# Optimization experiments

Hardware: AMD Instinct MI355X
Metric: run time of the kernel (lower is better)

## Reference

```python
import jax, jax.numpy as jnp
import numpy as np

B, T = 64, 1024
ATTN_DIM, RNN_DIM, ENC_DIM = 128, 1024, 512
N_FILT, KSIZE = 32, 31
PAD = (KSIZE - 1) // 2


def setup_inputs() -> dict:
    key = jax.random.key(0)
    ks = jax.random.split(key, 11)
    query = jax.random.normal(ks[0], (B, RNN_DIM), dtype=jnp.float32)
    keys = jax.random.normal(ks[1], (B, T, ENC_DIM), dtype=jnp.float32)
    values = jax.random.normal(ks[2], (B, T, ENC_DIM), dtype=jnp.float32)
    attention_weights_cum = jax.random.uniform(ks[3], (B, T), dtype=jnp.float32)
    mask = jnp.zeros((B, T), dtype=bool)
    s = 0.02
    W_loc_conv = jax.random.normal(ks[4], (N_FILT, 1, KSIZE), dtype=jnp.float32) * s
    W_loc_proj = jax.random.normal(ks[5], (ATTN_DIM, N_FILT), dtype=jnp.float32) * s
    W_query = jax.random.normal(ks[6], (ATTN_DIM, RNN_DIM), dtype=jnp.float32) * s
    W_key = jax.random.normal(ks[7], (ATTN_DIM, ENC_DIM), dtype=jnp.float32) * s
    W_value = jax.random.normal(ks[8], (ENC_DIM, ENC_DIM), dtype=jnp.float32) * s
    W_attn = jax.random.normal(ks[9], (1, ATTN_DIM), dtype=jnp.float32) * s
    return {
        "query": query, "keys": keys, "values": values,
        "attention_weights_cum": attention_weights_cum, "mask": mask,
        "W_loc_conv": W_loc_conv, "W_loc_proj": W_loc_proj,
        "W_query": W_query, "W_key": W_key, "W_value": W_value, "W_attn": W_attn,
    }


def reference(query, keys, values, attention_weights_cum, mask,
              W_loc_conv, W_loc_proj, W_query, W_key, W_value, W_attn):
    # location features: conv1d over cumulative attention, (B,1,T) -> (B,N_FILT,T)
    loc = jax.lax.conv_general_dilated(
        attention_weights_cum[:, None, :], W_loc_conv,
        window_strides=(1,), padding=[(PAD, PAD)],
        dimension_numbers=("NCH", "OIH", "NCH"))
    # (B,T,N_FILT) @ W_loc_proj.T -> (B,T,ATTN_DIM)
    loc_feat = jnp.einsum("bft,af->bta", loc, W_loc_proj)
    q_proj = query @ W_query.T                      # (B, ATTN_DIM)
    k_proj = jnp.einsum("bte,ae->bta", keys, W_key)  # (B, T, ATTN_DIM)
    energies = jnp.tanh(q_proj[:, None, :] + k_proj + loc_feat)
    scores = jnp.einsum("bta,a->bt", energies, W_attn[0])  # (B, T)
    scores = jnp.where(mask, -jnp.inf, scores)
    attn = jax.nn.softmax(scores, axis=-1)
    v_proj = jnp.einsum("bte,fe->btf", values, W_value)  # (B, T, ENC_DIM)
    context = jnp.einsum("bt,btf->bf", attn, v_proj)      # (B, ENC_DIM)
    return context, attn
```

## Files before the change

kernel.cpp:

```cpp
#include <hip/hip_runtime.h>
#include <math.h>

#define B_   64
#define T_   1024
#define AD   128
#define RD   1024
#define ED   512
#define NF   32
#define KS   31
#define PADW 15

typedef short bf16x8 __attribute__((ext_vector_type(8)));
typedef float f32x4  __attribute__((ext_vector_type(4)));

typedef __attribute__((address_space(1))) unsigned gu32;
typedef __attribute__((address_space(3))) unsigned lu32;

__device__ __forceinline__ void gll16(const void* g, void* l) {
  __builtin_amdgcn_global_load_lds(
      (gu32*)(unsigned long long)g,
      (lu32*)(unsigned)(unsigned long long)l, 16, 0, 0);
}

__device__ __forceinline__ short f2bf(float x) {
  union { float f; unsigned u; } v; v.f = x;
  unsigned r = (v.u + 0x7FFFu + ((v.u >> 16) & 1u)) >> 16;
  return (short)r;
}

__device__ __forceinline__ float tanh_fast(float x) {
  float t = __expf(2.0f * x);
  return (t - 1.0f) * __builtin_amdgcn_rcpf(t + 1.0f);
}

#define WAITV_(n)  asm volatile("s_waitcnt vmcnt(" #n ")" ::: "memory")
#define WAITV(n)   WAITV_(n)
#define WAITVL_(n) asm volatile("s_waitcnt vmcnt(" #n ") lgkmcnt(0)" ::: "memory")
#define WAITVL(n)  WAITVL_(n)
#define SB  __builtin_amdgcn_sched_barrier(0)
#define BAR __builtin_amdgcn_s_barrier()

__global__ __launch_bounds__(256) void prep_kernel(
    const float* __restrict__ Wk, const float* __restrict__ Wlp,
    const float* __restrict__ awc, const float* __restrict__ Wc,
    const float* __restrict__ query, const float* __restrict__ Wq,
    short* __restrict__ Wk16, short* __restrict__ Wlp16,
    short* __restrict__ loc_g, float* __restrict__ qp) {
  __shared__ float sh_awc[128 + KS - 1];
  __shared__ float sh_wc[NF * KS];
  __shared__ float sh_q[RD];
  __shared__ float sh_red[AD];
  const int blk = blockIdx.x, tid = threadIdx.x;

  if (blk < 68) {
    int p = blk * 256 + tid;
    const float* src; short* dst; int off;
    if (p < 16384) { src = Wk; dst = Wk16; off = p; }
    else           { src = Wlp; dst = Wlp16; off = p - 16384; }
    float4 v = *(const float4*)&src[off * 4];
    short4 h = { f2bf(v.x), f2bf(v.y), f2bf(v.z), f2bf(v.w) };
    *(short4*)&dst[off * 4] = h;
  } else if (blk < 68 + 512) {
    int cb = blk - 68;
    int b = cb >> 3, t0 = (cb & 7) * 128;
    for (int i = tid; i < NF * KS; i += 256) sh_wc[i] = Wc[i];
    if (tid < 128 + KS - 1) {
      int gt = t0 - PADW + tid;
      sh_awc[tid] = (gt >= 0 && gt < T_) ? awc[b * T_ + gt] : 0.0f;
    }
    __syncthreads();
    const int t = tid & 127, fh = (tid >> 7) * 16;
    for (int fq = 0; fq < 4; ++fq) {
      float s0 = 0.f, s1 = 0.f, s2 = 0.f, s3 = 0.f;
      const float* w0 = &sh_wc[(fh + fq * 4 + 0) * KS];
      const float* w1 = &sh_wc[(fh + fq * 4 + 1) * KS];
      const float* w2 = &sh_wc[(fh + fq * 4 + 2) * KS];
      const float* w3 = &sh_wc[(fh + fq * 4 + 3) * KS];
#pragma unroll
      for (int k = 0; k < KS; ++k) {
        float aw = sh_awc[t + k];
        s0 += w0[k] * aw; s1 += w1[k] * aw; s2 += w2[k] * aw; s3 += w3[k] * aw;
      }
      short4 h = { f2bf(s0), f2bf(s1), f2bf(s2), f2bf(s3) };
      *(short4*)&loc_g[((size_t)(b * T_ + t0 + t)) * NF + fh + fq * 4] = h;
    }
  } else {
    int b = blk - (68 + 512);
    *(float4*)&sh_q[tid * 4] = *(const float4*)&query[b * RD + tid * 4];
    __syncthreads();
    const int a = tid & 127, kh = tid >> 7;
    const float* wr = &Wq[(size_t)a * RD + kh * 512];
    const float* qr = &sh_q[kh * 512];
    float acc = 0.f;
    for (int e = 0; e < 512; e += 4) {
      float4 w = *(const float4*)&wr[e];
      acc += w.x * qr[e] + w.y * qr[e + 1] + w.z * qr[e + 2] + w.w * qr[e + 3];
    }
    if (kh == 1) sh_red[a] = acc;
    __syncthreads();
    if (kh == 0) qp[b * AD + a] = acc + sh_red[a];
  }
}

__global__ __launch_bounds__(256, 2) void scores_kernel(
    const float* __restrict__ keys, const short* __restrict__ Wk16,
    const short* __restrict__ Wlp16, const short* __restrict__ loc_g,
    const float* __restrict__ qp, const float* __restrict__ Wa,
    float* __restrict__ scores) {
  __shared__ alignas(16) short As[128 * 64];
  __shared__ alignas(16) short Bs[2][128 * 64];
  __shared__ float qp_s[AD], wa_s[AD];
  __shared__ float sc_s[128 * 2];

  const int tid = threadIdx.x;
  const int b = blockIdx.y, t0 = blockIdx.x * 128;
  const int lane = tid & 63, wave = tid >> 6;
  const int wm = wave >> 1, wn = wave & 1;
  const int m16 = lane & 15, s4 = lane >> 4;

  const int sr = tid >> 3;
  const int sg = tid & 7;
  const int swz = (sg ^ (sr & 7)) * 8;
  const float* kA = &keys[((size_t)(b * T_ + t0 + sr)) * ED + sg * 8];

  float4 bufA[8], bufB[8];
  auto LOADA = [&](float4 (&buf)[8], int kc) {
#pragma unroll
    for (int i = 0; i < 4; ++i) {
      const float* p = kA + (size_t)i * 32 * ED + (size_t)kc * 64;
      buf[2 * i]     = *(const float4*)p;
      buf[2 * i + 1] = *(const float4*)(p + 4);
    }
  };
  auto WRITEA = [&](float4 (&buf)[8]) {
#pragma unroll
    for (int i = 0; i < 4; ++i) {
      bf16x8 h = { f2bf(buf[2*i].x),   f2bf(buf[2*i].y),
                   f2bf(buf[2*i].z),   f2bf(buf[2*i].w),
                   f2bf(buf[2*i+1].x), f2bf(buf[2*i+1].y),
                   f2bf(buf[2*i+1].z), f2bf(buf[2*i+1].w) };
      *(bf16x8*)&As[(sr + i * 32) * 64 + swz] = h;
    }
  };

  const int r8 = lane >> 3, cb8 = lane & 7;
  const int cbg = cb8 ^ r8;
  auto STAGEB = [&](int kc, int half) {
#pragma unroll
    for (int i = 0; i < 4; ++i) {
      int row = wave * 32 + i * 8;
      gll16(&Wk16[(size_t)(row + r8) * ED + (size_t)kc * 64 + cbg * 8],
            &Bs[half][row * 64]);
    }
  };
  f32x4 acc[4][4];
  auto COMPUTE = [&](int half) {
#pragma unroll
    for (int kk2 = 0; kk2 < 2; ++kk2) {
      const int j = kk2 * 4 + s4;
      const int ca = (j ^ (m16 & 7)) * 8;
      bf16x8 af[4], bfr[4];
#pragma unroll
      for (int mt = 0; mt < 4; ++mt)
        af[mt] = *(const bf16x8*)&As[(wm * 64 + mt * 16 + m16) * 64 + ca];
#pragma unroll
      for (int nt = 0; nt < 4; ++nt)
        bfr[nt] = *(const bf16x8*)&Bs[half][(wn * 64 + nt * 16 + m16) * 64 + ca];
      __builtin_amdgcn_s_setprio(1);
#pragma unroll
      for (int mt = 0; mt < 4; ++mt)
#pragma unroll
        for (int nt = 0; nt < 4; ++nt)
          acc[mt][nt] = __builtin_amdgcn_mfma_f32_16x16x32_bf16(
              af[mt], bfr[nt], acc[mt][nt], 0, 0, 0);
      __builtin_amdgcn_s_setprio(0);
    }
  };

  if (tid < AD) qp_s[tid] = qp[b * AD + tid];
  else          wa_s[tid - AD] = Wa[tid - AD];
  SB;
  {
    const int r = lane >> 2, cbl = lane & 3;
#pragma unroll
    for (int i = 0; i < 2; ++i) {
      int row = wave * 32 + i * 16;
      gll16(&loc_g[((size_t)(b * T_ + t0 + row + r)) * NF + cbl * 8],
            &As[row * 32]);
      gll16(&Wlp16[(row + r) * NF + cbl * 8], &Bs[1][row * 32]);
    }
  }
  SB;
  LOADA(bufA, 0); SB;
  STAGEB(0, 0);   SB;
  LOADA(bufB, 1); SB;
  WAITVL(20);
  SB; BAR; SB;

  {
    bf16x8 af[4], bfr[4];
#pragma unroll
    for (int mt = 0; mt < 4; ++mt)
      af[mt] = *(const bf16x8*)&As[(wm * 64 + mt * 16 + m16) * 32 + s4 * 8];
#pragma unroll
    for (int nt = 0; nt < 4; ++nt)
      bfr[nt] = *(const bf16x8*)&Bs[1][(wn * 64 + nt * 16 + m16) * 32 + s4 * 8];
#pragma unroll
    for (int mt = 0; mt < 4; ++mt)
#pragma unroll
      for (int nt = 0; nt < 4; ++nt)
        acc[mt][nt] = __builtin_amdgcn_mfma_f32_16x16x32_bf16(
            af[mt], bfr[nt], (f32x4){0.f, 0.f, 0.f, 0.f}, 0, 0, 0);
  }

#define CHUNK(i, BUF, PRE, MID, DOG, DOL)                    \
  do {                                                       \
    BAR; SB;           \
    WAITV(PRE); SB;                     \
    WRITEA(BUF); SB;                                         \
    if (DOG) STAGEB((i) + 1, ((i) + 1) & 1);                 \
    SB;                                                      \
    if (DOL) LOADA(BUF, (i) + 2);                            \
    SB;                                                      \
    WAITVL(MID);            \
    SB; BAR; SB;                                             \
    COMPUTE((i) & 1);                                        \
  } while (0)

  CHUNK(0, bufA, 12, 20, true,  true);
  CHUNK(1, bufB, 12, 20, true,  true);
  CHUNK(2, bufA, 12, 20, true,  true);
  CHUNK(3, bufB, 12, 20, true,  true);
  CHUNK(4, bufA, 12, 20, true,  true);
  CHUNK(5, bufB, 12, 20, true,  true);
  CHUNK(6, bufA, 12, 12, true,  false);
  CHUNK(7, bufB,  4,  0, false, false);
#undef CHUNK

  __syncthreads();

  float qv[4], wv[4];
#pragma unroll
  for (int nt = 0; nt < 4; ++nt) {
    int a = wn * 64 + nt * 16 + m16;
    qv[nt] = qp_s[a]; wv[nt] = wa_s[a];
  }
#pragma unroll
  for (int mt = 0; mt < 4; ++mt) {
#pragma unroll
    for (int r = 0; r < 4; ++r) {
      float p = 0.f;
#pragma unroll
      for (int nt = 0; nt < 4; ++nt)
        p += wv[nt] * tanh_fast(acc[mt][nt][r] + qv[nt]);
      p += __shfl_xor(p, 1); p += __shfl_xor(p, 2);
      p += __shfl_xor(p, 4); p += __shfl_xor(p, 8);
      if (m16 == 0) sc_s[(wm * 64 + mt * 16 + s4 * 4 + r) * 2 + wn] = p;
    }
  }
  __syncthreads();
  if (tid < 128)
    scores[(size_t)b * T_ + t0 + tid] = sc_s[tid * 2] + sc_s[tid * 2 + 1];
}

__global__ __launch_bounds__(256) void softmax_kernel(
    const float* __restrict__ scores, const unsigned char* __restrict__ mask,
    float* __restrict__ attn) {
  const int b = blockIdx.x, tid = threadIdx.x;
  __shared__ float redm[4], reds[4];

  float4 s4 = *(const float4*)&scores[b * T_ + tid * 4];
  uchar4 m4 = *(const uchar4*)&mask[b * T_ + tid * 4];
  if (m4.x) s4.x = -INFINITY;
  if (m4.y) s4.y = -INFINITY;
  if (m4.z) s4.z = -INFINITY;
  if (m4.w) s4.w = -INFINITY;

  float mx = fmaxf(fmaxf(s4.x, s4.y), fmaxf(s4.z, s4.w));
#pragma unroll
  for (int off = 32; off >= 1; off >>= 1) mx = fmaxf(mx, __shfl_xor(mx, off, 64));
  if ((tid & 63) == 0) redm[tid >> 6] = mx;
  __syncthreads();
  mx = fmaxf(fmaxf(redm[0], redm[1]), fmaxf(redm[2], redm[3]));

  float e0 = expf(s4.x - mx), e1 = expf(s4.y - mx);
  float e2 = expf(s4.z - mx), e3 = expf(s4.w - mx);
  float sum = e0 + e1 + e2 + e3;
#pragma unroll
  for (int off = 32; off >= 1; off >>= 1) sum += __shfl_xor(sum, off, 64);
  if ((tid & 63) == 0) reds[tid >> 6] = sum;
  __syncthreads();
  sum = reds[0] + reds[1] + reds[2] + reds[3];

  float inv = 1.0f / sum;
  float4 o4 = { e0 * inv, e1 * inv, e2 * inv, e3 * inv };
  *(float4*)&attn[b * T_ + tid * 4] = o4;
}

__global__ __launch_bounds__(256) void wvsum_kernel(
    const float* __restrict__ values, const float* __restrict__ attn,
    float* __restrict__ wvp) {
  const int tc = blockIdx.x, b = blockIdx.y, tid = threadIdx.x;
  __shared__ float at_s[32];
  if (tid < 32) at_s[tid] = attn[b * T_ + tc * 32 + tid];
  __syncthreads();
  const int e4 = tid & 127, th = tid >> 7;
  const float* vb =
      values + ((size_t)(b * T_ + tc * 32 + th * 16)) * ED + e4 * 4;
  const float* as = &at_s[th * 16];
  float4 acc = {0.f, 0.f, 0.f, 0.f};
#pragma unroll
  for (int t8 = 0; t8 < 16; t8 += 8) {
    float4 v[8];
#pragma unroll
    for (int u = 0; u < 8; ++u)
      v[u] = *(const float4*)&vb[(size_t)(t8 + u) * ED];
#pragma unroll
    for (int u = 0; u < 8; ++u) {
      float a = as[t8 + u];
      acc.x = fmaf(a, v[u].x, acc.x); acc.y = fmaf(a, v[u].y, acc.y);
      acc.z = fmaf(a, v[u].z, acc.z); acc.w = fmaf(a, v[u].w, acc.w);
    }
  }
  *(float4*)&wvp[((size_t)(b * 64 + tc * 2 + th)) * ED + e4 * 4] = acc;
}

__global__ __launch_bounds__(256) void context_kernel(
    const float* __restrict__ wvp, const float* __restrict__ Wv,
    float* __restrict__ ctx) {
  const int fq = blockIdx.x, b = blockIdx.y, tid = threadIdx.x;
  __shared__ float wv_s[ED];
  __shared__ float red[128];
  for (int e = tid; e < ED; e += 256) {
    float s = 0.f;
    const float* base = &wvp[(size_t)b * 64 * ED + e];
#pragma unroll 16
    for (int p = 0; p < 64; ++p) s += base[p * ED];
    wv_s[e] = s;
  }
  __syncthreads();
  const int fl = tid & 127, eh = tid >> 7;
  const int f = fq * 128 + fl;
  const float* wr = &Wv[(size_t)f * ED + eh * 256];
  const float* qr = &wv_s[eh * 256];
  float acc = 0.f;
  for (int e = 0; e < 256; e += 4) {
    float4 w = *(const float4*)&wr[e];
    acc += w.x * qr[e] + w.y * qr[e + 1] + w.z * qr[e + 2] + w.w * qr[e + 3];
  }
  if (eh == 1) red[fl] = acc;
  __syncthreads();
  if (eh == 0) ctx[b * ED + f] = acc + red[fl];
}

extern "C" void kernel_launch(void* const* d_in, const int* in_sizes, int n_in,
                              void* d_out, int out_size, void* d_ws, size_t ws_size,
                              hipStream_t stream) {
  const float* query = (const float*)d_in[0];
  const float* keys  = (const float*)d_in[1];
  const float* values= (const float*)d_in[2];
  const float* awc   = (const float*)d_in[3];
  const unsigned char* mask = (const unsigned char*)d_in[4];
  const float* Wc    = (const float*)d_in[5];
  const float* Wlp   = (const float*)d_in[6];
  const float* Wq    = (const float*)d_in[7];
  const float* Wk    = (const float*)d_in[8];
  const float* Wv    = (const float*)d_in[9];
  const float* Wa    = (const float*)d_in[10];

  float* ctx  = (float*)d_out;
  float* attn = (float*)d_out + B_ * ED;

  float* ws = (float*)d_ws;
  float* qp      = ws;
  float* scoresB = qp + B_ * AD;
  float* wvp     = scoresB + B_ * T_;
  short* Wk16    = (short*)(wvp + (size_t)B_ * 64 * ED);
  short* Wlp16   = Wk16 + AD * ED;
  short* loc_g   = Wlp16 + AD * NF;

  prep_kernel<<<68 + 512 + 64, 256, 0, stream>>>(Wk, Wlp, awc, Wc, query, Wq,
                                                 Wk16, Wlp16, loc_g, qp);
  scores_kernel<<<dim3(8, B_), 256, 0, stream>>>(keys, Wk16, Wlp16, loc_g,
                                                 qp, Wa, scoresB);
  softmax_kernel<<<B_, 256, 0, stream>>>(scoresB, mask, attn);
  wvsum_kernel<<<dim3(32, B_), 256, 0, stream>>>(values, attn, wvp);
  context_kernel<<<dim3(4, B_), 256, 0, stream>>>(wvp, Wv, ctx);
}
```

Baseline: 338.4 us.

## Fuse softmax into scores and context into wvsum via last-block counters

Removes the separate softmax and context kernels. The last scores block for each batch, found with an atomic counter, computes the softmax. The weighted value sum now uses 8 blocks per batch that each cover 128 timesteps, with register double-buffered loads. Partial sums are combined by float atomics into a per-batch buffer, and the last block applies Wv to produce the context. This cuts two launches and the large wvp intermediate, at the cost of serial tail work in a single block per batch, fewer blocks for the value pass, and nondeterministic float atomic ordering.

```diff
diff --git a/kernel.cpp b/kernel.cpp
--- a/kernel.cpp
+++ b/kernel.cpp
@@ -45,7 +45,9 @@
     const float* __restrict__ awc, const float* __restrict__ Wc,
     const float* __restrict__ query, const float* __restrict__ Wq,
     short* __restrict__ Wk16, short* __restrict__ Wlp16,
-    short* __restrict__ loc_g, float* __restrict__ qp) {
+    short* __restrict__ loc_g, float* __restrict__ qp,
+    float* __restrict__ yb, int* __restrict__ cnt_sm,
+    int* __restrict__ cnt_wv) {
   __shared__ float sh_awc[128 + KS - 1];
   __shared__ float sh_wc[NF * KS];
   __shared__ float sh_q[RD];
@@ -86,6 +88,10 @@
     }
   } else {
     int b = blk - (68 + 512);
+    if (tid < 128) *(float4*)&yb[(size_t)b * ED + tid * 4] =
+        (float4){0.f, 0.f, 0.f, 0.f};
+    if (tid == 254) cnt_sm[b] = 0;
+    if (tid == 255) cnt_wv[b] = 0;
     *(float4*)&sh_q[tid * 4] = *(const float4*)&query[b * RD + tid * 4];
     __syncthreads();
     const int a = tid & 127, kh = tid >> 7;
@@ -106,11 +112,14 @@
     const float* __restrict__ keys, const short* __restrict__ Wk16,
     const short* __restrict__ Wlp16, const short* __restrict__ loc_g,
     const float* __restrict__ qp, const float* __restrict__ Wa,
-    float* __restrict__ scores) {
+    const unsigned char* __restrict__ mask, float* __restrict__ scores,
+    float* __restrict__ attn, int* __restrict__ cnt_sm) {
   __shared__ alignas(16) short As[128 * 64];
   __shared__ alignas(16) short Bs[2][128 * 64];
   __shared__ float qp_s[AD], wa_s[AD];
   __shared__ float sc_s[128 * 2];
+  __shared__ float redm[4], reds[4];
+  __shared__ int lastf;
 
   const int tid = threadIdx.x;
   const int b = blockIdx.y, t0 = blockIdx.x * 128;
@@ -261,30 +270,30 @@
   __syncthreads();
   if (tid < 128)
     scores[(size_t)b * T_ + t0 + tid] = sc_s[tid * 2] + sc_s[tid * 2 + 1];
-}
-
-__global__ __launch_bounds__(256) void softmax_kernel(
-    const float* __restrict__ scores, const unsigned char* __restrict__ mask,
-    float* __restrict__ attn) {
-  const int b = blockIdx.x, tid = threadIdx.x;
-  __shared__ float redm[4], reds[4];
-
-  float4 s4 = *(const float4*)&scores[b * T_ + tid * 4];
+
+  __threadfence();
+  __syncthreads();
+  if (tid == 0) lastf = (atomicAdd(&cnt_sm[b], 1) == 7) ? 1 : 0;
+  __syncthreads();
+  if (!lastf) return;
+  __threadfence();
+
+  float4 s4v = *(const float4*)&scores[(size_t)b * T_ + tid * 4];
   uchar4 m4 = *(const uchar4*)&mask[b * T_ + tid * 4];
-  if (m4.x) s4.x = -INFINITY;
-  if (m4.y) s4.y = -INFINITY;
-  if (m4.z) s4.z = -INFINITY;
-  if (m4.w) s4.w = -INFINITY;
-
-  float mx = fmaxf(fmaxf(s4.x, s4.y), fmaxf(s4.z, s4.w));
+  if (m4.x) s4v.x = -INFINITY;
+  if (m4.y) s4v.y = -INFINITY;
+  if (m4.z) s4v.z = -INFINITY;
+  if (m4.w) s4v.w = -INFINITY;
+
+  float mx = fmaxf(fmaxf(s4v.x, s4v.y), fmaxf(s4v.z, s4v.w));
 #pragma unroll
   for (int off = 32; off >= 1; off >>= 1) mx = fmaxf(mx, __shfl_xor(mx, off, 64));
   if ((tid & 63) == 0) redm[tid >> 6] = mx;
   __syncthreads();
   mx = fmaxf(fmaxf(redm[0], redm[1]), fmaxf(redm[2], redm[3]));
 
-  float e0 = expf(s4.x - mx), e1 = expf(s4.y - mx);
-  float e2 = expf(s4.z - mx), e3 = expf(s4.w - mx);
+  float e0 = expf(s4v.x - mx), e1 = expf(s4v.y - mx);
+  float e2 = expf(s4v.z - mx), e3 = expf(s4v.w - mx);
   float sum = e0 + e1 + e2 + e3;
 #pragma unroll
   for (int off = 32; off >= 1; off >>= 1) sum += __shfl_xor(sum, off, 64);
@@ -297,60 +306,79 @@
   *(float4*)&attn[b * T_ + tid * 4] = o4;
 }
 
-__global__ __launch_bounds__(256) void wvsum_kernel(
+__global__ __launch_bounds__(256) void wvctx_kernel(
     const float* __restrict__ values, const float* __restrict__ attn,
-    float* __restrict__ wvp) {
+    const float* __restrict__ Wv, float* __restrict__ yb,
+    int* __restrict__ cnt_wv, float* __restrict__ ctx) {
   const int tc = blockIdx.x, b = blockIdx.y, tid = threadIdx.x;
-  __shared__ float at_s[32];
-  if (tid < 32) at_s[tid] = attn[b * T_ + tc * 32 + tid];
-  __syncthreads();
+  __shared__ float at_s[128];
+  __shared__ float4 red[128];
+  __shared__ float y_s[ED];
+  __shared__ int lastw;
+
+  if (tid < 128) at_s[tid] = attn[b * T_ + tc * 128 + tid];
+  __syncthreads();
+
   const int e4 = tid & 127, th = tid >> 7;
   const float* vb =
-      values + ((size_t)(b * T_ + tc * 32 + th * 16)) * ED + e4 * 4;
-  const float* as = &at_s[th * 16];
+      values + ((size_t)(b * T_ + tc * 128 + th * 64)) * ED + e4 * 4;
+  const float* as = &at_s[th * 64];
+
   float4 acc = {0.f, 0.f, 0.f, 0.f};
-#pragma unroll
-  for (int t8 = 0; t8 < 16; t8 += 8) {
-    float4 v[8];
-#pragma unroll
-    for (int u = 0; u < 8; ++u)
-      v[u] = *(const float4*)&vb[(size_t)(t8 + u) * ED];
+  float4 cur[8], nxt[8];
+#pragma unroll
+  for (int u = 0; u < 8; ++u) cur[u] = *(const float4*)&vb[(size_t)u * ED];
+#pragma unroll
+  for (int t8 = 0; t8 < 64; t8 += 8) {
+    if (t8 + 8 < 64) {
+#pragma unroll
+      for (int u = 0; u < 8; ++u)
+        nxt[u] = *(const float4*)&vb[(size_t)(t8 + 8 + u) * ED];
+    }
 #pragma unroll
     for (int u = 0; u < 8; ++u) {
       float a = as[t8 + u];
-      acc.x = fmaf(a, v[u].x, acc.x); acc.y = fmaf(a, v[u].y, acc.y);
-      acc.z = fmaf(a, v[u].z, acc.z); acc.w = fmaf(a, v[u].w, acc.w);
-    }
-  }
-  *(float4*)&wvp[((size_t)(b * 64 + tc * 2 + th)) * ED + e4 * 4] = acc;
-}
-
-__global__ __launch_bounds__(256) void context_kernel(
-    const float* __restrict__ wvp, const float* __restrict__ Wv,
-    float* __restrict__ ctx) {
-  const int fq = blockIdx.x, b = blockIdx.y, tid = threadIdx.x;
-  __shared__ float wv_s[ED];
-  __shared__ float red[128];
-  for (int e = tid; e < ED; e += 256) {
-    float s = 0.f;
-    const float* base = &wvp[(size_t)b * 64 * ED + e];
-#pragma unroll 16
-    for (int p = 0; p < 64; ++p) s += base[p * ED];
-    wv_s[e] = s;
-  }
-  __syncthreads();
-  const int fl = tid & 127, eh = tid >> 7;
-  const int f = fq * 128 + fl;
-  const float* wr = &Wv[(size_t)f * ED + eh * 256];
-  const float* qr = &wv_s[eh * 256];
-  float acc = 0.f;
-  for (int e = 0; e < 256; e += 4) {
-    float4 w = *(const float4*)&wr[e];
-    acc += w.x * qr[e] + w.y * qr[e + 1] + w.z * qr[e + 2] + w.w * qr[e + 3];
-  }
-  if (eh == 1) red[fl] = acc;
-  __syncthreads();
-  if (eh == 0) ctx[b * ED + f] = acc + red[fl];
+      acc.x = fmaf(a, cur[u].x, acc.x); acc.y = fmaf(a, cur[u].y, acc.y);
+      acc.z = fmaf(a, cur[u].z, acc.z); acc.w = fmaf(a, cur[u].w, acc.w);
+    }
+#pragma unroll
+    for (int u = 0; u < 8; ++u) cur[u] = nxt[u];
+  }
+
+  if (th == 1) red[e4] = acc;
+  __syncthreads();
+  if (th == 0) {
+    float4 r = red[e4];
+    acc.x += r.x; acc.y += r.y; acc.z += r.z; acc.w += r.w;
+    float* yp = &yb[(size_t)b * ED + e4 * 4];
+    atomicAdd(yp + 0, acc.x); atomicAdd(yp + 1, acc.y);
+    atomicAdd(yp + 2, acc.z); atomicAdd(yp + 3, acc.w);
+  }
+
+  __threadfence();
+  __syncthreads();
+  if (tid == 0) lastw = (atomicAdd(&cnt_wv[b], 1) == 7) ? 1 : 0;
+  __syncthreads();
+  if (!lastw) return;
+  __threadfence();
+
+  if (tid < 128)
+    *(float4*)&y_s[tid * 4] = *(const float4*)&yb[(size_t)b * ED + tid * 4];
+  __syncthreads();
+
+  const int f0 = tid * 2;
+  const float* w0 = &Wv[(size_t)f0 * ED];
+  const float* w1 = w0 + ED;
+  float a0 = 0.f, a1 = 0.f;
+  for (int e = 0; e < ED; e += 4) {
+    float4 y = *(const float4*)&y_s[e];
+    float4 wA = *(const float4*)&w0[e];
+    float4 wB = *(const float4*)&w1[e];
+    a0 += wA.x * y.x + wA.y * y.y + wA.z * y.z + wA.w * y.w;
+    a1 += wB.x * y.x + wB.y * y.y + wB.z * y.z + wB.w * y.w;
+  }
+  ctx[(size_t)b * ED + f0]     = a0;
+  ctx[(size_t)b * ED + f0 + 1] = a1;
 }
 
 extern "C" void kernel_launch(void* const* d_in, const int* in_sizes, int n_in,
@@ -374,16 +402,17 @@
   float* ws = (float*)d_ws;
   float* qp      = ws;
   float* scoresB = qp + B_ * AD;
-  float* wvp     = scoresB + B_ * T_;
-  short* Wk16    = (short*)(wvp + (size_t)B_ * 64 * ED);
+  float* yb      = scoresB + B_ * T_;
+  int*   cnt_sm  = (int*)(yb + B_ * ED);
+  int*   cnt_wv  = cnt_sm + 64;
+  short* Wk16    = (short*)(cnt_sm + 128);
   short* Wlp16   = Wk16 + AD * ED;
   short* loc_g   = Wlp16 + AD * NF;
 
-  prep_kernel<<<68 + 512 + 64, 256, 0, stream>>>(Wk, Wlp, awc, Wc, query, Wq,
-                                                 Wk16, Wlp16, loc_g, qp);
-  scores_kernel<<<dim3(8, B_), 256, 0, stream>>>(keys, Wk16, Wlp16, loc_g,
-                                                 qp, Wa, scoresB);
-  softmax_kernel<<<B_, 256, 0, stream>>>(scoresB, mask, attn);
-  wvsum_kernel<<<dim3(32, B_), 256, 0, stream>>>(values, attn, wvp);
-  context_kernel<<<dim3(4, B_), 256, 0, stream>>>(wvp, Wv, ctx);
-}
+  prep_kernel<<<68 + 512 + 64, 256, 0, stream>>>(
+      Wk, Wlp, awc, Wc, query, Wq, Wk16, Wlp16, loc_g, qp, yb, cnt_sm, cnt_wv);
+  scores_kernel<<<dim3(8, B_), 256, 0, stream>>>(
+      keys, Wk16, Wlp16, loc_g, qp, Wa, mask, scoresB, attn, cnt_sm);
+  wvctx_kernel<<<dim3(8, B_), 256, 0, stream>>>(values, attn, Wv, yb, cnt_wv,
+                                                ctx);
+}
```

New measurement: 528.4 us. 1.56x slower.
